# Kernel tuning notes

Measured on AMD Instinct MI355X. Metric: run time of the kernel, lower is better.

The kernel has to match this reference:

```python
import jax, jax.numpy as jnp
import numpy as np

N_NODES = 20000
N_RAND_EDGES = 160000
X_DIM, Z_DIM, H, D = 256, 64, 8, 128


def setup_inputs() -> dict:
    key = jax.random.key(0)
    ks = jax.random.split(key, 12)
    x = jax.random.normal(ks[0], (N_NODES, X_DIM), dtype=jnp.float32)
    W = jax.random.normal(ks[1], (X_DIM, H * D), dtype=jnp.float32) * (X_DIM ** -0.5)
    attn_l = jax.random.normal(ks[2], (H, D), dtype=jnp.float32) * (D ** -0.5)
    attn_r = jax.random.normal(ks[3], (H, D), dtype=jnp.float32) * (D ** -0.5)
    res_W = jax.random.normal(ks[4], (X_DIM, H * D), dtype=jnp.float32) * (X_DIM ** -0.5)
    bias = jnp.zeros((H * D,), dtype=jnp.float32)
    gamma = jnp.ones((D,), dtype=jnp.float32)
    beta = jnp.zeros((D,), dtype=jnp.float32)
    mu_W = jax.random.normal(ks[5], (D, Z_DIM), dtype=jnp.float32) * (D ** -0.5)
    mu_b = jnp.zeros((Z_DIM,), dtype=jnp.float32)
    ls_W = jax.random.normal(ks[6], (D, Z_DIM), dtype=jnp.float32) * (D ** -0.5)
    ls_b = jnp.zeros((Z_DIM,), dtype=jnp.float32)
    # random edges + self loops (dgl.add_self_loop)
    loops = jnp.arange(N_NODES, dtype=jnp.int64)
    src = jnp.concatenate([jax.random.randint(ks[7], (N_RAND_EDGES,), 0, N_NODES).astype(jnp.int64), loops])
    dst = jnp.concatenate([jax.random.randint(ks[8], (N_RAND_EDGES,), 0, N_NODES).astype(jnp.int64), loops])
    return {"x": x, "W": W, "attn_l": attn_l, "attn_r": attn_r, "res_W": res_W,
            "bias": bias, "gamma": gamma, "beta": beta, "mu_W": mu_W, "mu_b": mu_b,
            "ls_W": ls_W, "ls_b": ls_b, "src": src, "dst": dst}


def reference(x, W, attn_l, attn_r, res_W, bias, gamma, beta, mu_W, mu_b, ls_W, ls_b, src, dst):
    N = x.shape[0]
    # GATConv: shared linear projection -> [N, H, D]
    feat = (x @ W).reshape(N, H, D)
    el = jnp.einsum('nhd,hd->nh', feat, attn_l)  # [N, H]
    er = jnp.einsum('nhd,hd->nh', feat, attn_r)
    # per-edge attention logits, LeakyReLU(0.2)
    e = jax.nn.leaky_relu(el[src] + er[dst], negative_slope=0.2)  # [E, H]
    # segment softmax over incoming edges of each destination node
    m = jax.ops.segment_max(e, dst, num_segments=N)
    a = jnp.exp(e - m[dst])
    s = jax.ops.segment_sum(a, dst, num_segments=N)
    alpha = a / s[dst]  # [E, H] (attn_drop disabled: eval-mode deterministic)
    # weighted scatter-aggregation
    rst = jax.ops.segment_sum(feat[src] * alpha[:, :, None], dst, num_segments=N)  # [N,H,D]
    # residual projection (in_feats != H*D -> linear res_fc, no bias) + conv bias
    rst = rst + (x @ res_W).reshape(N, H, D) + bias.reshape(H, D)
    # head-sum -> ReLU -> BatchNorm1d (training stats, biased var) ; dropout disabled
    h = jax.nn.relu(rst.sum(axis=1))  # [N, 128]
    mean = h.mean(axis=0)
    var = h.var(axis=0)
    h = (h - mean) * jax.lax.rsqrt(var + 1e-5) * gamma + beta
    mu = h @ mu_W + mu_b
    log_sigma = jnp.clip(h @ ls_W + ls_b, -10.0, 10.0)
    return mu, log_sigma
```

## Files before the change

### kernel.cpp

```cpp
#include <hip/hip_runtime.h>
#include <hip/hip_bf16.h>

#define XD 256
#define HH 8
#define DD 128
#define ZD 64
#define CAP 64
#define AGGB 2560
#define REDB 64
#define LOG2E 1.44269504088896340736f

using f32x4 = __attribute__((ext_vector_type(4))) float;
using s16x8 = __attribute__((ext_vector_type(8))) short;

static __device__ __forceinline__ float bf2f(unsigned short u) {
    union { unsigned int i; float f; } v; v.i = ((unsigned int)u) << 16; return v.f;
}
static __device__ __forceinline__ unsigned short f2bf(float f) {
    union { float f; unsigned int i; } v; v.f = f;
    unsigned int r = v.i + 0x7FFFu + ((v.i >> 16) & 1u);
    return (unsigned short)(r >> 16);
}
static __device__ __forceinline__ void gload_lds16(const void* g, void* l) {
    __builtin_amdgcn_global_load_lds(
        (const __attribute__((address_space(1))) unsigned int*)g,
        (__attribute__((address_space(3))) unsigned int*)l, 16, 0, 0);
}
static __device__ __forceinline__ void fatomic_add(float* p, float v) {
    __hip_atomic_fetch_add(p, v, __ATOMIC_RELAXED, __HIP_MEMORY_SCOPE_AGENT);
}

__global__ void prep_kernel(const float* __restrict__ x, const float* __restrict__ W,
                            const float* __restrict__ resW, const float* __restrict__ bias,
                            unsigned short* __restrict__ xb, unsigned short* __restrict__ wtb,
                            unsigned short* __restrict__ rwtb, float* __restrict__ bias_sum,
                            int N, int NPAD) {
    long long i = (long long)blockIdx.x * blockDim.x + threadIdx.x;
    long long nx4 = (long long)NPAD * XD / 4;
    if (i < nx4) {
        long long e = i * 4;
        long long lim = (long long)N * XD;
        float4 v = {0.f, 0.f, 0.f, 0.f};
        if (e < lim) v = *(const float4*)(x + e);
        ushort4 o; o.x = f2bf(v.x); o.y = f2bf(v.y); o.z = f2bf(v.z); o.w = f2bf(v.w);
        *(ushort4*)(xb + e) = o;
        return;
    }
    i -= nx4;
    if (i < XD * HH * DD) {
        int col = (int)(i >> 8), k = (int)(i & 255);
        wtb[i] = f2bf(W[(long long)k * (HH * DD) + col]);
        return;
    }
    i -= XD * HH * DD;
    if (i < DD * XD) {
        int d = (int)(i >> 8), k = (int)(i & 255);
        float s = 0.f;
        #pragma unroll
        for (int h = 0; h < HH; ++h) s += resW[(long long)k * (HH * DD) + h * DD + d];
        rwtb[i] = f2bf(s);
        return;
    }
    i -= DD * XD;
    if (i < DD) {
        float s = 0.f;
        #pragma unroll
        for (int h = 0; h < HH; ++h) s += bias[h * DD + (int)i];
        bias_sum[i] = s;
    }
}

__global__ __launch_bounds__(256) void gemm1_kernel(
    const unsigned short* __restrict__ xb,
    const unsigned short* __restrict__ wtb,
    const unsigned short* __restrict__ rwtb,
    const float* __restrict__ attn_l, const float* __restrict__ attn_r,
    unsigned short* __restrict__ featb,
    float* __restrict__ hres,
    float* __restrict__ el, float* __restrict__ er,
    int N) {
    __shared__ unsigned short As[128 * 64];
    __shared__ unsigned short Bs[128 * 64];
    const int tid = threadIdx.x;
    const int lane = tid & 63;
    const int wid = tid >> 6;
    const int wm = wid >> 1, wn = wid & 1;
    const int brow = blockIdx.x * 128;
    const int y = blockIdx.y;
    const unsigned short* bsrc = (y < 8) ? (wtb + y * 128 * 256) : rwtb;

    f32x4 acc[4][4] = {};
    for (int kt = 0; kt < 4; ++kt) {
        #pragma unroll
        for (int it = 0; it < 4; ++it) {
            int c = it * 256 + tid;
            int row = c >> 3, kc = c & 7;
            gload_lds16(xb  + (brow + row) * 256 + kt * 64 + kc * 8, (char*)As + c * 16);
            gload_lds16(bsrc + row * 256 + kt * 64 + kc * 8,          (char*)Bs + c * 16);
        }
        __syncthreads();
        #pragma unroll
        for (int ks = 0; ks < 2; ++ks) {
            s16x8 a[4], b[4];
            #pragma unroll
            for (int m = 0; m < 4; ++m)
                a[m] = *(const s16x8*)(As + (wm * 64 + m * 16 + (lane & 15)) * 64 + ks * 32 + (lane >> 4) * 8);
            #pragma unroll
            for (int n = 0; n < 4; ++n)
                b[n] = *(const s16x8*)(Bs + (wn * 64 + n * 16 + (lane & 15)) * 64 + ks * 32 + (lane >> 4) * 8);
            #pragma unroll
            for (int m = 0; m < 4; ++m)
                #pragma unroll
                for (int n = 0; n < 4; ++n)
                    acc[m][n] = __builtin_amdgcn_mfma_f32_16x16x32_bf16(a[m], b[n], acc[m][n], 0, 0, 0);
        }
        __syncthreads();
    }

    if (y < 8) {
        float al[4], ar[4];
        #pragma unroll
        for (int n = 0; n < 4; ++n) {
            int colh = wn * 64 + n * 16 + (lane & 15);
            al[n] = attn_l[y * 128 + colh] * LOG2E;
            ar[n] = attn_r[y * 128 + colh] * LOG2E;
        }
        #pragma unroll
        for (int m = 0; m < 4; ++m) {
            #pragma unroll
            for (int j = 0; j < 4; ++j) {
                int row = brow + wm * 64 + m * 16 + (lane >> 4) * 4 + j;
                float pel = 0.f, per = 0.f;
                #pragma unroll
                for (int n = 0; n < 4; ++n) { pel += acc[m][n][j] * al[n]; per += acc[m][n][j] * ar[n]; }
                #pragma unroll
                for (int o = 1; o < 16; o <<= 1) { pel += __shfl_xor(pel, o); per += __shfl_xor(per, o); }
                if ((lane & 15) == 0 && row < N) {
                    fatomic_add(el + row * 8 + y, pel);
                    fatomic_add(er + row * 8 + y, per);
                }
            }
        }
        #pragma unroll
        for (int m = 0; m < 4; ++m)
            #pragma unroll
            for (int n = 0; n < 4; ++n)
                #pragma unroll
                for (int j = 0; j < 4; ++j) {
                    int row = brow + wm * 64 + m * 16 + (lane >> 4) * 4 + j;
                    if (row < N) {
                        int col = y * 128 + wn * 64 + n * 16 + (lane & 15);
                        featb[(long long)row * 1024 + col] = f2bf(acc[m][n][j]);
                    }
                }
    } else {
        #pragma unroll
        for (int m = 0; m < 4; ++m)
            #pragma unroll
            for (int n = 0; n < 4; ++n)
                #pragma unroll
                for (int j = 0; j < 4; ++j) {
                    int row = brow + wm * 64 + m * 16 + (lane >> 4) * 4 + j;
                    if (row < N) {
                        int col = wn * 64 + n * 16 + (lane & 15);
                        hres[(long long)row * 128 + col] = acc[m][n][j];
                    }
                }
    }
}

__global__ void bucket_kernel(const int* __restrict__ src, const int* __restrict__ dst,
                              int* __restrict__ cnt, int* __restrict__ bucket, int E) {
    int e = blockIdx.x * blockDim.x + threadIdx.x;
    if (e >= E) return;
    int sN = src[e], dN = dst[e];
    int idx = atomicAdd(cnt + dN, 1);
    if (idx < CAP) bucket[dN * CAP + idx] = sN;
}

__global__ __launch_bounds__(256) void agg_kernel(
    const unsigned short* __restrict__ featb,
    const float* __restrict__ el, const float* __restrict__ er,
    const int* __restrict__ cnt, const int* __restrict__ bucket,
    const float* __restrict__ hres, const float* __restrict__ bias_sum,
    unsigned short* __restrict__ hbf, float* __restrict__ partial, int N) {
    const int lane = threadIdx.x & 63;
    const int wv = threadIdx.x >> 6;
    const int d0 = lane * 2;
    float psum0 = 0.f, psq0 = 0.f, psum1 = 0.f, psq1 = 0.f;
    for (int n = blockIdx.x * 4 + wv; n < N; n += gridDim.x * 4) {
        float4 er0 = *(const float4*)(er + n * 8);
        float4 er1 = *(const float4*)(er + n * 8 + 4);
        float erv[8] = {er0.x, er0.y, er0.z, er0.w, er1.x, er1.y, er1.z, er1.w};
        int c = cnt[n]; if (c > CAP) c = CAP;
        float sden[8] = {0.f, 0.f, 0.f, 0.f, 0.f, 0.f, 0.f, 0.f};
        float a0h[8] = {0.f, 0.f, 0.f, 0.f, 0.f, 0.f, 0.f, 0.f};
        float a1h[8] = {0.f, 0.f, 0.f, 0.f, 0.f, 0.f, 0.f, 0.f};
        int s_nx = 0;
        if (c > 0) s_nx = bucket[n * CAP];
        for (int i = 0; i < c; ++i) {
            int sn = s_nx;
            if (i + 1 < c) s_nx = bucket[n * CAP + i + 1];
            float4 el0 = *(const float4*)(el + sn * 8);
            float4 el1 = *(const float4*)(el + sn * 8 + 4);
            float elv[8] = {el0.x, el0.y, el0.z, el0.w, el1.x, el1.y, el1.z, el1.w};
            float wh[8];
            #pragma unroll
            for (int h = 0; h < 8; ++h) {
                float v = elv[h] + erv[h];
                v = fmaxf(v, 0.2f * v);
                wh[h] = __builtin_exp2f(v);
                sden[h] += wh[h];
            }
            const unsigned short* fb = featb + (long long)sn * 1024 + d0;
            #pragma unroll
            for (int h = 0; h < 8; ++h) {
                unsigned int u = *(const unsigned int*)(fb + h * 128);
                union { unsigned int i; float f; } cl, ch;
                cl.i = u << 16;
                ch.i = u & 0xffff0000u;
                a0h[h] += wh[h] * cl.f;
                a1h[h] += wh[h] * ch.f;
            }
        }
        float a0 = 0.f, a1 = 0.f;
        #pragma unroll
        for (int h = 0; h < 8; ++h) {
            float inv = 1.f / sden[h];
            a0 += a0h[h] * inv;
            a1 += a1h[h] * inv;
        }
        float h0 = a0 + hres[n * 128 + d0]     + bias_sum[d0];
        float h1 = a1 + hres[n * 128 + d0 + 1] + bias_sum[d0 + 1];
        h0 = h0 > 0.f ? h0 : 0.f;
        h1 = h1 > 0.f ? h1 : 0.f;
        unsigned int pack = (unsigned int)f2bf(h0) | ((unsigned int)f2bf(h1) << 16);
        *(unsigned int*)(hbf + (long long)n * 128 + d0) = pack;
        psum0 += h0; psq0 += h0 * h0; psum1 += h1; psq1 += h1 * h1;
    }
    __shared__ float red[4][64][4];
    red[wv][lane][0] = psum0; red[wv][lane][1] = psq0;
    red[wv][lane][2] = psum1; red[wv][lane][3] = psq1;
    __syncthreads();
    if (wv == 0) {
        float t0 = 0.f, t1 = 0.f, t2 = 0.f, t3 = 0.f;
        #pragma unroll
        for (int k = 0; k < 4; ++k) {
            t0 += red[k][lane][0]; t1 += red[k][lane][1];
            t2 += red[k][lane][2]; t3 += red[k][lane][3];
        }
        *(float4*)(partial + (blockIdx.x * 64 + lane) * 4) = make_float4(t0, t1, t2, t3);
    }
}

__global__ __launch_bounds__(256) void reduce_kernel(const float* __restrict__ partial,
                                                     float* __restrict__ fin, int nblk) {
    const int t = threadIdx.x;
    const int rows = (nblk + gridDim.x - 1) / gridDim.x;
    const int b0 = blockIdx.x * rows;
    float a0 = 0.f, a1 = 0.f, a2 = 0.f, a3 = 0.f;
    for (int u = 0; u + 3 < rows; u += 4) {
        int bb = b0 + u;
        if (bb + 3 < nblk) {
            a0 += partial[(long long)bb * 256 + t];
            a1 += partial[(long long)(bb + 1) * 256 + t];
            a2 += partial[(long long)(bb + 2) * 256 + t];
            a3 += partial[(long long)(bb + 3) * 256 + t];
        } else {
            for (int k = 0; k < 4 && bb + k < nblk; ++k) a0 += partial[(long long)(bb + k) * 256 + t];
        }
    }
    for (int u = rows & ~3; u < rows; ++u)
        if (b0 + u < nblk) a0 += partial[(long long)(b0 + u) * 256 + t];
    fatomic_add(fin + t, (a0 + a1) + (a2 + a3));
}

__global__ __launch_bounds__(1024) void fold_kernel(
    const float* __restrict__ fin,
    const float* __restrict__ gamma, const float* __restrict__ beta,
    const float* __restrict__ muW, const float* __restrict__ mub,
    const float* __restrict__ lsW, const float* __restrict__ lsb,
    unsigned short* __restrict__ wcat, float* __restrict__ bcat, int N) {
    __shared__ float sc_s[128], sh_s[128];
    __shared__ float redA[1024];
    const int t = threadIdx.x;
    if (t < 128) {
        float sum = fin[(t >> 1) * 4 + (t & 1) * 2];
        float sq  = fin[(t >> 1) * 4 + (t & 1) * 2 + 1];
        float mean = sum / (float)N;
        float var = sq / (float)N - mean * mean;
        float rs = rsqrtf(var + 1e-5f);
        float sc = rs * gamma[t];
        sc_s[t] = sc;
        sh_s[t] = beta[t] - mean * sc;
    }
    __syncthreads();
    for (int i = t; i < 128 * 128; i += 1024) {
        int cc = i >> 7, d = i & 127;
        float wsrc = (cc < 64) ? muW[d * 64 + cc] : lsW[d * 64 + (cc - 64)];
        wcat[i] = f2bf(sc_s[d] * wsrc);
    }
    {
        int cc = t & 127, dc = t >> 7;
        float a = 0.f;
        #pragma unroll
        for (int u = 0; u < 16; ++u) {
            int d = dc * 16 + u;
            float wsrc = (cc < 64) ? muW[d * 64 + cc] : lsW[d * 64 + (cc - 64)];
            a += sh_s[d] * wsrc;
        }
        redA[t] = a;
    }
    __syncthreads();
    if (t < 128) {
        float b = (t < 64) ? mub[t] : lsb[t - 64];
        #pragma unroll
        for (int k = 0; k < 8; ++k) b += redA[k * 128 + t];
        bcat[t] = b;
    }
}

__global__ __launch_bounds__(256) void outgemm_kernel(
    const unsigned short* __restrict__ hbf,
    const unsigned short* __restrict__ wcat,
    const float* __restrict__ bcat,
    float* __restrict__ out, int N) {
    __shared__ unsigned short As[128 * 64];
    __shared__ unsigned short Bs[128 * 64];
    const int tid = threadIdx.x;
    const int lane = tid & 63;
    const int wid = tid >> 6;
    const int wm = wid >> 1, wn = wid & 1;
    const int brow = blockIdx.x * 128;

    f32x4 acc[4][4] = {};
    for (int kt = 0; kt < 2; ++kt) {
        #pragma unroll
        for (int it = 0; it < 4; ++it) {
            int c = it * 256 + tid;
            int row = c >> 3, kc = c & 7;
            gload_lds16(hbf + (brow + row) * 128 + kt * 64 + kc * 8, (char*)As + c * 16);
            gload_lds16(wcat + row * 128 + kt * 64 + kc * 8,          (char*)Bs + c * 16);
        }
        __syncthreads();
        #pragma unroll
        for (int ks = 0; ks < 2; ++ks) {
            s16x8 a[4], b[4];
            #pragma unroll
            for (int m = 0; m < 4; ++m)
                a[m] = *(const s16x8*)(As + (wm * 64 + m * 16 + (lane & 15)) * 64 + ks * 32 + (lane >> 4) * 8);
            #pragma unroll
            for (int n = 0; n < 4; ++n)
                b[n] = *(const s16x8*)(Bs + (wn * 64 + n * 16 + (lane & 15)) * 64 + ks * 32 + (lane >> 4) * 8);
            #pragma unroll
            for (int m = 0; m < 4; ++m)
                #pragma unroll
                for (int n = 0; n < 4; ++n)
                    acc[m][n] = __builtin_amdgcn_mfma_f32_16x16x32_bf16(a[m], b[n], acc[m][n], 0, 0, 0);
        }
        __syncthreads();
    }

    float bc[4];
    #pragma unroll
    for (int n = 0; n < 4; ++n) bc[n] = bcat[wn * 64 + n * 16 + (lane & 15)];
    #pragma unroll
    for (int m = 0; m < 4; ++m)
        #pragma unroll
        for (int n = 0; n < 4; ++n) {
            int col = wn * 64 + n * 16 + (lane & 15);
            #pragma unroll
            for (int j = 0; j < 4; ++j) {
                int row = brow + wm * 64 + m * 16 + (lane >> 4) * 4 + j;
                if (row < N) {
                    float v = acc[m][n][j] + bc[n];
                    if (col < 64) {
                        out[(long long)row * 64 + col] = v;
                    } else {
                        v = fminf(fmaxf(v, -10.f), 10.f);
                        out[(long long)N * 64 + (long long)row * 64 + (col - 64)] = v;
                    }
                }
            }
        }
}

extern "C" void kernel_launch(void* const* d_in, const int* in_sizes, int n_in,
                              void* d_out, int out_size, void* d_ws, size_t ws_size,
                              hipStream_t stream) {
    const float* x      = (const float*)d_in[0];
    const float* W      = (const float*)d_in[1];
    const float* attn_l = (const float*)d_in[2];
    const float* attn_r = (const float*)d_in[3];
    const float* resW   = (const float*)d_in[4];
    const float* bias   = (const float*)d_in[5];
    const float* gamma  = (const float*)d_in[6];
    const float* beta   = (const float*)d_in[7];
    const float* muW    = (const float*)d_in[8];
    const float* mub    = (const float*)d_in[9];
    const float* lsW    = (const float*)d_in[10];
    const float* lsb    = (const float*)d_in[11];
    const int*   src    = (const int*)d_in[12];
    const int*   dst    = (const int*)d_in[13];

    const int N = in_sizes[0] / XD;
    const int E = in_sizes[12];
    const int NPAD = ((N + 127) / 128) * 128;

    char* p = (char*)d_ws;
    size_t off = 0;
    auto alloc = [&](size_t bytes) -> void* {
        void* r = p + off;
        off = (off + bytes + 255) & ~(size_t)255;
        return r;
    };
    unsigned short* xb   = (unsigned short*)alloc((size_t)NPAD * XD * 2);
    unsigned short* wtb  = (unsigned short*)alloc((size_t)XD * HH * DD * 2);
    unsigned short* rwtb = (unsigned short*)alloc((size_t)DD * XD * 2);
    float* bias_sum      = (float*)alloc(DD * 4);
    unsigned short* featb= (unsigned short*)alloc((size_t)N * HH * DD * 2);
    float* hres          = (float*)alloc((size_t)N * DD * 4);
    float* el            = (float*)alloc((size_t)N * HH * 4);
    float* er            = (float*)alloc((size_t)N * HH * 4);
    int*   cnt           = (int*)alloc((size_t)N * 4);
    float* fin           = (float*)alloc(256 * 4);
    int*   bucket        = (int*)alloc((size_t)N * CAP * 4);
    unsigned short* hbf  = (unsigned short*)alloc((size_t)NPAD * DD * 2);
    float* partial       = (float*)alloc((size_t)AGGB * 256 * 4);
    unsigned short* wcat = (unsigned short*)alloc(128 * 128 * 2);
    float* bcat          = (float*)alloc(128 * 4);

    size_t zbytes = (size_t)((char*)bucket - (char*)el);
    hipMemsetAsync(el, 0, zbytes, stream);

    long long prep_total = (long long)NPAD * XD / 4 + XD * HH * DD + DD * XD + DD;
    int prep_blocks = (int)((prep_total + 255) / 256);
    prep_kernel<<<prep_blocks, 256, 0, stream>>>(x, W, resW, bias, xb, wtb, rwtb, bias_sum, N, NPAD);

    dim3 g1(NPAD / 128, HH + 1);
    gemm1_kernel<<<g1, 256, 0, stream>>>(xb, wtb, rwtb, attn_l, attn_r, featb, hres, el, er, N);

    bucket_kernel<<<(E + 255) / 256, 256, 0, stream>>>(src, dst, cnt, bucket, E);

    agg_kernel<<<AGGB, 256, 0, stream>>>(featb, el, er, cnt, bucket, hres, bias_sum,
                                         hbf, partial, N);

    reduce_kernel<<<REDB, 256, 0, stream>>>(partial, fin, AGGB);

    fold_kernel<<<1, 1024, 0, stream>>>(fin, gamma, beta, muW, mub, lsW, lsb, wcat, bcat, N);

    outgemm_kernel<<<NPAD / 128, 256, 0, stream>>>(hbf, wcat, bcat, (float*)d_out, N);
}
```

Baseline: 252.7 us.

## Remap aggregation lanes to head-major 16-element chunks with cross-lane head reduction

The aggregation kernel now gives each lane one head and a 16-element chunk of the feature row. Lanes issue two 16-byte loads per edge instead of eight 4-byte loads, and each lane computes one exp instead of eight. The per-head partial sums are then combined across lanes with xor shuffles and redistributed through shared memory. The change also prefetches the next edge's features and halves the aggregation grid, at the cost of more registers per lane and extra shuffle and LDS traffic per node.

```diff
diff --git a/kernel.cpp b/kernel.cpp
--- a/kernel.cpp
+++ b/kernel.cpp
@@ -6,7 +6,7 @@
 #define DD 128
 #define ZD 64
 #define CAP 64
-#define AGGB 2560
+#define AGGB 1280
 #define REDB 64
 #define LOG2E 1.44269504088896340736f
 
@@ -186,59 +186,84 @@
     unsigned short* __restrict__ hbf, float* __restrict__ partial, int N) {
     const int lane = threadIdx.x & 63;
     const int wv = threadIdx.x >> 6;
+    const int hh = lane >> 3;
+    const int cc = lane & 7;
     const int d0 = lane * 2;
+    __shared__ float hsh[4][128];
+    __shared__ float red[4][64][4];
     float psum0 = 0.f, psq0 = 0.f, psum1 = 0.f, psq1 = 0.f;
     for (int n = blockIdx.x * 4 + wv; n < N; n += gridDim.x * 4) {
-        float4 er0 = *(const float4*)(er + n * 8);
-        float4 er1 = *(const float4*)(er + n * 8 + 4);
-        float erv[8] = {er0.x, er0.y, er0.z, er0.w, er1.x, er1.y, er1.z, er1.w};
+        const float erv = er[n * 8 + hh];
         int c = cnt[n]; if (c > CAP) c = CAP;
-        float sden[8] = {0.f, 0.f, 0.f, 0.f, 0.f, 0.f, 0.f, 0.f};
-        float a0h[8] = {0.f, 0.f, 0.f, 0.f, 0.f, 0.f, 0.f, 0.f};
-        float a1h[8] = {0.f, 0.f, 0.f, 0.f, 0.f, 0.f, 0.f, 0.f};
-        int s_nx = 0;
-        if (c > 0) s_nx = bucket[n * CAP];
+        float sden = 0.f;
+        float acc[16];
+        #pragma unroll
+        for (int k = 0; k < 16; ++k) acc[k] = 0.f;
+        uint4 f0n = {0,0,0,0}, f1n = {0,0,0,0};
+        float eln = 0.f;
+        if (c > 0) {
+            int sn0 = bucket[n * CAP];
+            const unsigned short* fb = featb + (long long)sn0 * 1024 + hh * 128 + cc * 16;
+            f0n = *(const uint4*)(fb);
+            f1n = *(const uint4*)(fb + 8);
+            eln = el[sn0 * 8 + hh];
+        }
         for (int i = 0; i < c; ++i) {
-            int sn = s_nx;
-            if (i + 1 < c) s_nx = bucket[n * CAP + i + 1];
-            float4 el0 = *(const float4*)(el + sn * 8);
-            float4 el1 = *(const float4*)(el + sn * 8 + 4);
-            float elv[8] = {el0.x, el0.y, el0.z, el0.w, el1.x, el1.y, el1.z, el1.w};
-            float wh[8];
-            #pragma unroll
-            for (int h = 0; h < 8; ++h) {
-                float v = elv[h] + erv[h];
-                v = fmaxf(v, 0.2f * v);
-                wh[h] = __builtin_exp2f(v);
-                sden[h] += wh[h];
+            uint4 f0 = f0n, f1 = f1n;
+            float elv = eln;
+            if (i + 1 < c) {
+                int sn2 = bucket[n * CAP + i + 1];
+                const unsigned short* fb2 = featb + (long long)sn2 * 1024 + hh * 128 + cc * 16;
+                f0n = *(const uint4*)(fb2);
+                f1n = *(const uint4*)(fb2 + 8);
+                eln = el[sn2 * 8 + hh];
             }
-            const unsigned short* fb = featb + (long long)sn * 1024 + d0;
-            #pragma unroll
-            for (int h = 0; h < 8; ++h) {
-                unsigned int u = *(const unsigned int*)(fb + h * 128);
-                union { unsigned int i; float f; } cl, ch;
-                cl.i = u << 16;
-                ch.i = u & 0xffff0000u;
-                a0h[h] += wh[h] * cl.f;
-                a1h[h] += wh[h] * ch.f;
-            }
-        }
-        float a0 = 0.f, a1 = 0.f;
-        #pragma unroll
-        for (int h = 0; h < 8; ++h) {
-            float inv = 1.f / sden[h];
-            a0 += a0h[h] * inv;
-            a1 += a1h[h] * inv;
-        }
-        float h0 = a0 + hres[n * 128 + d0]     + bias_sum[d0];
-        float h1 = a1 + hres[n * 128 + d0 + 1] + bias_sum[d0 + 1];
+            float v = elv + erv;
+            v = fmaxf(v, 0.2f * v);
+            float w = __builtin_exp2f(v);
+            sden += w;
+            unsigned int uu0 = f0.x, uu1 = f0.y, uu2 = f0.z, uu3 = f0.w;
+            unsigned int uu4 = f1.x, uu5 = f1.y, uu6 = f1.z, uu7 = f1.w;
+            union { unsigned int i; float f; } t;
+            t.i = uu0 << 16;        acc[0]  += w * t.f;
+            t.i = uu0 & 0xffff0000u; acc[1]  += w * t.f;
+            t.i = uu1 << 16;        acc[2]  += w * t.f;
+            t.i = uu1 & 0xffff0000u; acc[3]  += w * t.f;
+            t.i = uu2 << 16;        acc[4]  += w * t.f;
+            t.i = uu2 & 0xffff0000u; acc[5]  += w * t.f;
+            t.i = uu3 << 16;        acc[6]  += w * t.f;
+            t.i = uu3 & 0xffff0000u; acc[7]  += w * t.f;
+            t.i = uu4 << 16;        acc[8]  += w * t.f;
+            t.i = uu4 & 0xffff0000u; acc[9]  += w * t.f;
+            t.i = uu5 << 16;        acc[10] += w * t.f;
+            t.i = uu5 & 0xffff0000u; acc[11] += w * t.f;
+            t.i = uu6 << 16;        acc[12] += w * t.f;
+            t.i = uu6 & 0xffff0000u; acc[13] += w * t.f;
+            t.i = uu7 << 16;        acc[14] += w * t.f;
+            t.i = uu7 & 0xffff0000u; acc[15] += w * t.f;
+        }
+        float inv = (c > 0) ? (1.f / sden) : 0.f;
+        #pragma unroll
+        for (int k = 0; k < 16; ++k) acc[k] *= inv;
+        #pragma unroll
+        for (int off = 8; off <= 32; off <<= 1) {
+            #pragma unroll
+            for (int k = 0; k < 16; ++k) acc[k] += __shfl_xor(acc[k], off, 64);
+        }
+        if (hh == 0) {
+            #pragma unroll
+            for (int k = 0; k < 16; ++k) hsh[wv][cc * 16 + k] = acc[k];
+        }
+        __builtin_amdgcn_wave_barrier();
+        float h0 = hsh[wv][d0]     + hres[(long long)n * 128 + d0]     + bias_sum[d0];
+        float h1 = hsh[wv][d0 + 1] + hres[(long long)n * 128 + d0 + 1] + bias_sum[d0 + 1];
+        __builtin_amdgcn_wave_barrier();
         h0 = h0 > 0.f ? h0 : 0.f;
         h1 = h1 > 0.f ? h1 : 0.f;
         unsigned int pack = (unsigned int)f2bf(h0) | ((unsigned int)f2bf(h1) << 16);
         *(unsigned int*)(hbf + (long long)n * 128 + d0) = pack;
         psum0 += h0; psq0 += h0 * h0; psum1 += h1; psq1 += h1 * h1;
     }
-    __shared__ float red[4][64][4];
     red[wv][lane][0] = psum0; red[wv][lane][1] = psq0;
     red[wv][lane][2] = psum1; red[wv][lane][3] = psq1;
     __syncthreads();
```

After: 251.2 us. About the same (-0.6%).
